# Performance work log

Hardware: AMD Instinct MI355X
Metric: run time of the kernel (lower is better)

The kernel has to match this reference:

```python
import jax, jax.numpy as jnp
import numpy as np

VOCAB, EMB, HID = 1000, 128, 256
B, T = 64, 1024


def setup_inputs() -> dict:
    key = jax.random.key(0)
    k1, k2, k3, k4, k5, k6, k7 = jax.random.split(key, 7)
    loading_lists = jax.random.randint(k1, (B, T), 0, VOCAB)
    lengths = jnp.maximum(jax.random.randint(k2, (B,), 0, T), 1)  # length >= 1 as in env
    s_ih = 1.0 / np.sqrt(HID)
    return {
        "loading_lists": loading_lists,
        "loading_list_lengths": lengths,
        "emb": jax.random.normal(k3, (VOCAB, EMB), dtype=jnp.float32),
        "W_ih": jax.random.uniform(k4, (4 * HID, EMB), minval=-s_ih, maxval=s_ih, dtype=jnp.float32),
        "W_hh": jax.random.uniform(k5, (4 * HID, HID), minval=-s_ih, maxval=s_ih, dtype=jnp.float32),
        "b_ih": jax.random.uniform(k6, (4 * HID,), minval=-s_ih, maxval=s_ih, dtype=jnp.float32),
        "b_hh": jax.random.uniform(k7, (4 * HID,), minval=-s_ih, maxval=s_ih, dtype=jnp.float32),
    }


def reference(loading_lists, loading_list_lengths, emb, W_ih, W_hh, b_ih, b_hh):
    # Embedding lookup: [B, T, E]
    x = emb[loading_lists]
    Bv, Tv, _ = x.shape
    H = W_hh.shape[1]
    # Precompute input projections for all timesteps: [B, T, 4H]
    xproj = jnp.einsum("bte,ge->btg", x, W_ih) + b_ih + b_hh
    xproj_t = jnp.swapaxes(xproj, 0, 1)  # [T, B, 4H]
    lengths = loading_list_lengths

    def step(carry, inp):
        h, c = carry
        xw_t, t = inp
        gates = xw_t + h @ W_hh.T  # [B, 4H]
        i_g, f_g, g_g, o_g = jnp.split(gates, 4, axis=-1)  # torch gate order i,f,g,o
        i_g = jax.nn.sigmoid(i_g)
        f_g = jax.nn.sigmoid(f_g)
        g_g = jnp.tanh(g_g)
        o_g = jax.nn.sigmoid(o_g)
        c_new = f_g * c + i_g * g_g
        h_new = o_g * jnp.tanh(c_new)
        valid = (t < lengths)[:, None]  # freeze state past each sample's length
        h = jnp.where(valid, h_new, h)
        c = jnp.where(valid, c_new, c)
        return (h, c), None

    h0 = jnp.zeros((Bv, H), dtype=x.dtype)
    c0 = jnp.zeros((Bv, H), dtype=x.dtype)
    (h_last, _), _ = jax.lax.scan(step, (h0, c0), (xproj_t, jnp.arange(Tv)))
    return h_last  # [B, H]
```

## Files before the change

kernel.cpp:

```cpp
#include <hip/hip_runtime.h>
#include <math.h>

#define VOCAB 1000
#define EMB   128
#define HID   256
#define G4    1024
#define BATCH 64
#define SEQT  1024
#define KVH   48
#define KLH   16

typedef unsigned int u32;
typedef _Float16 f16;
typedef __attribute__((ext_vector_type(2))) _Float16 h2v;
union H2U { u32 u; h2v h; unsigned short s[2]; };

#if defined(__has_builtin)
# if __has_builtin(__builtin_amdgcn_fdot2)
#  define HAVE_FDOT2 1
# endif
#endif
__device__ __forceinline__ float fdot2_(u32 a, u32 b, float c) {
    H2U ua, ub; ua.u = a; ub.u = b;
#ifdef HAVE_FDOT2
    return __builtin_amdgcn_fdot2(ua.h, ub.h, c, false);
#else
    return c + (float)ua.h.x * (float)ub.h.x + (float)ua.h.y * (float)ub.h.y;
#endif
}

__device__ __forceinline__ float sigmoidf_(float x) {
    return 1.f / (1.f + __expf(-x));
}
__device__ __forceinline__ float tanhf_(float x) {
    return 1.f - 2.f / (__expf(2.f * x) + 1.f);
}

__global__ __launch_bounds__(1024) void eproj_kernel(
    const float* __restrict__ emb, const float* __restrict__ W_ih,
    const float* __restrict__ b_ih, const float* __restrict__ b_hh,
    float* __restrict__ eproj)
{
    const int v0 = blockIdx.x * 8;
    const int g  = threadIdx.x;
    __shared__ __align__(16) float4 x_sh[8][EMB / 4];
    if (g < 256) {
        const int r = g >> 5, cc = g & 31;
        x_sh[r][cc] = ((const float4*)(emb + (size_t)(v0 + r) * EMB))[cc];
    }
    __syncthreads();
    const float4* wrow = (const float4*)(W_ih + (size_t)g * EMB);
    float a0[8], a1[8], a2[8], a3[8];
#pragma unroll
    for (int r = 0; r < 8; r++) { a0[r] = a1[r] = a2[r] = a3[r] = 0.f; }
#pragma unroll 4
    for (int e4 = 0; e4 < EMB / 4; e4++) {
        float4 wv = wrow[e4];
#pragma unroll
        for (int r = 0; r < 8; r++) {
            float4 xv = x_sh[r][e4];
            a0[r] += wv.x * xv.x;
            a1[r] += wv.y * xv.y;
            a2[r] += wv.z * xv.z;
            a3[r] += wv.w * xv.w;
        }
    }
    const float bias = b_ih[g] + b_hh[g];
#pragma unroll
    for (int r = 0; r < 8; r++)
        eproj[(size_t)(v0 + r) * G4 + g] =
            (a0[r] + a1[r]) + (a2[r] + a3[r]) + bias;
}

__global__ __launch_bounds__(128) void pack_whh(
    const float* __restrict__ Whh, u32* __restrict__ wvq, u32* __restrict__ wlq)
{
    const int r = blockIdx.x;
    const int m = threadIdx.x;
    H2U u;
    u.h.x = (f16)Whh[(size_t)r * HID + 2 * m];
    u.h.y = (f16)Whh[(size_t)r * HID + 2 * m + 1];
    const int j  = m >> 6;
    const int mm = m & 63;
    if (mm < KVH) {
        const int chunk = j * (KVH / 4) + (mm >> 2);
        wvq[(size_t)chunk * (G4 * 4) + r * 4 + (mm & 3)] = u.u;
    } else {
        const int t2 = mm - KVH;
        const int chunk = j * (KLH / 4) + (t2 >> 2);
        wlq[(size_t)chunk * (G4 * 4) + r * 4 + (t2 & 3)] = u.u;
    }
}

#define REG_CHUNK(q) do {                                                   \
    uint4 h4 = hb4[(q)];                                                    \
    aI = fdot2_(wI[4*(q)+0], h4.x, aI); aF = fdot2_(wF[4*(q)+0], h4.x, aF); \
    aG = fdot2_(wG[4*(q)+0], h4.x, aG); aO = fdot2_(wO[4*(q)+0], h4.x, aO); \
    aI = fdot2_(wI[4*(q)+1], h4.y, aI); aF = fdot2_(wF[4*(q)+1], h4.y, aF); \
    aG = fdot2_(wG[4*(q)+1], h4.y, aG); aO = fdot2_(wO[4*(q)+1], h4.y, aO); \
    aI = fdot2_(wI[4*(q)+2], h4.z, aI); aF = fdot2_(wF[4*(q)+2], h4.z, aF); \
    aG = fdot2_(wG[4*(q)+2], h4.z, aG); aO = fdot2_(wO[4*(q)+2], h4.z, aO); \
    aI = fdot2_(wI[4*(q)+3], h4.w, aI); aF = fdot2_(wF[4*(q)+3], h4.w, aF); \
    aG = fdot2_(wG[4*(q)+3], h4.w, aG); aO = fdot2_(wO[4*(q)+3], h4.w, aO); \
} while (0)

#define TAIL_CHUNK(q) do {                                                  \
    uint4 h4 = hb4[KVH / 4 + (q)];                                          \
    const int ch = j * (KLH / 4) + (q);                                     \
    uint4 tI = ((const uint4*)wl_sh)[ch * G4 + rI];                         \
    uint4 tF = ((const uint4*)wl_sh)[ch * G4 + rF];                         \
    uint4 tG = ((const uint4*)wl_sh)[ch * G4 + rG];                         \
    uint4 tO = ((const uint4*)wl_sh)[ch * G4 + rO];                         \
    aI = fdot2_(tI.x, h4.x, aI); aF = fdot2_(tF.x, h4.x, aF);               \
    aG = fdot2_(tG.x, h4.x, aG); aO = fdot2_(tO.x, h4.x, aO);               \
    aI = fdot2_(tI.y, h4.y, aI); aF = fdot2_(tF.y, h4.y, aF);               \
    aG = fdot2_(tG.y, h4.y, aG); aO = fdot2_(tO.y, h4.y, aO);               \
    aI = fdot2_(tI.z, h4.z, aI); aF = fdot2_(tF.z, h4.z, aF);               \
    aG = fdot2_(tG.z, h4.z, aG); aO = fdot2_(tO.z, h4.z, aO);               \
    aI = fdot2_(tI.w, h4.w, aI); aF = fdot2_(tF.w, h4.w, aF);               \
    aG = fdot2_(tG.w, h4.w, aG); aO = fdot2_(tO.w, h4.w, aO);               \
} while (0)

__global__ __launch_bounds__(512, 2) void lstm_single_cu(
    const int* __restrict__ ids, const int* __restrict__ lens,
    const float* __restrict__ eproj,
    const u32* __restrict__ wvq, const u32* __restrict__ wlq,
    float* __restrict__ out)
{
    const int b   = blockIdx.x;
    const int tau = threadIdx.x;
    const int u   = tau & (HID - 1);
    const int j   = tau >> 8;
    const int rI  = u;
    const int rF  = 256 + u;
    const int rG  = 512 + u;
    const int rO  = 768 + u;

    __shared__ u32    wl_sh[2 * (KLH / 4) * G4 * 4];
    __shared__ u32    h2_sh[2][HID / 2];
    __shared__ float4 gs4[HID];
    __shared__ int    id_sh[SEQT];

    const int* idr = ids + (size_t)b * SEQT;
    ((int2*)id_sh)[tau] = ((const int2*)idr)[tau];
    if (tau < HID / 2) h2_sh[0][tau] = 0u;

    {
        const uint4* src = (const uint4*)wlq;
        uint4*       dst = (uint4*)wl_sh;
#pragma unroll
        for (int t = 0; t < 2 * (KLH / 4) * G4 / 512; t++)
            dst[t * 512 + tau] = src[t * 512 + tau];
    }

    u32 wI[KVH], wF[KVH], wG[KVH], wO[KVH];
#pragma unroll
    for (int q = 0; q < KVH / 4; q++) {
        const int ch = j * (KVH / 4) + q;
        uint4 ti = ((const uint4*)wvq)[ch * G4 + rI];
        uint4 tf = ((const uint4*)wvq)[ch * G4 + rF];
        uint4 tg = ((const uint4*)wvq)[ch * G4 + rG];
        uint4 to = ((const uint4*)wvq)[ch * G4 + rO];
        wI[4 * q + 0] = ti.x; wI[4 * q + 1] = ti.y;
        wI[4 * q + 2] = ti.z; wI[4 * q + 3] = ti.w;
        wF[4 * q + 0] = tf.x; wF[4 * q + 1] = tf.y;
        wF[4 * q + 2] = tf.z; wF[4 * q + 3] = tf.w;
        wG[4 * q + 0] = tg.x; wG[4 * q + 1] = tg.y;
        wG[4 * q + 2] = tg.z; wG[4 * q + 3] = tg.w;
        wO[4 * q + 0] = to.x; wO[4 * q + 1] = to.y;
        wO[4 * q + 2] = to.z; wO[4 * q + 3] = to.w;
    }

    const int len = lens[b];
    float c = 0.f, hf = 0.f;

    float xI = 0.f, xF = 0.f, xG = 0.f, xO = 0.f;
    if (j == 0) {
        const float* e0 = eproj + (size_t)idr[0] * G4;
        xI = e0[rI]; xF = e0[rF]; xG = e0[rG]; xO = e0[rO];
    }

    __syncthreads();

    for (int t = 0; t < len; t++) {
        const int nt = (t + 1 < len) ? t + 1 : len - 1;
        const int nid = id_sh[nt];
        float nI = 0.f, nF = 0.f, nG = 0.f, nO = 0.f;
        if (j == 0) {
            const float* en = eproj + (size_t)nid * G4;
            nI = en[rI]; nF = en[rF]; nG = en[rG]; nO = en[rO];
        }

        const int p = t & 1;
        const uint4* hb4 = (const uint4*)h2_sh[p] + 16 * j;
        float aI = xI, aF = xF, aG = xG, aO = xO;

        if (j == 0) {
#pragma unroll
            for (int q = 0; q < KVH / 4; q++) REG_CHUNK(q);
#pragma unroll
            for (int q = 0; q < KLH / 4; q++) TAIL_CHUNK(q);
        } else {
#pragma unroll
            for (int q = 0; q < KLH / 4; q++) TAIL_CHUNK(q);
#pragma unroll
            for (int q = 0; q < KVH / 4; q++) REG_CHUNK(q);
        }

        if (j == 1) {
            gs4[u] = make_float4(aI, aF, aG, aO);
        }
        __syncthreads();

        if (j == 0) {
            float4 pp = gs4[u];
            float ig = sigmoidf_(aI + pp.x);
            float fg = sigmoidf_(aF + pp.y);
            float gg = tanhf_(aG + pp.z);
            float og = sigmoidf_(aO + pp.w);
            c  = fg * c + ig * gg;
            hf = og * tanhf_(c);
            H2U hv; hv.h.x = (f16)hf; hv.h.y = (f16)0.f;
            ((unsigned short*)h2_sh[p ^ 1])[u] = hv.s[0];
        }
        xI = nI; xF = nF; xG = nG; xO = nO;
        __syncthreads();
    }

    if (tau < HID) out[(size_t)b * HID + u] = hf;
}

__global__ __launch_bounds__(1024, 1) void lstm_fallback(
    const int* __restrict__ ids, const int* __restrict__ lens,
    const float* __restrict__ emb, const float* __restrict__ W_ih,
    const float* __restrict__ b_ih, const float* __restrict__ b_hh,
    const float* __restrict__ W_hh, float* __restrict__ out)
{
    const int b = blockIdx.x;
    const int t = threadIdx.x;

    __shared__ __align__(16) float h_sh[HID];
    __shared__ __align__(16) float c_sh[HID];
    __shared__ __align__(16) float gates[G4];
    __shared__ __align__(16) float x_sh[EMB];

    float wih[EMB];
    {
        const float4* wr = (const float4*)(W_ih + (size_t)t * EMB);
#pragma unroll
        for (int e4 = 0; e4 < EMB / 4; e4++) {
            float4 wv = wr[e4];
            wih[4 * e4 + 0] = wv.x;
            wih[4 * e4 + 1] = wv.y;
            wih[4 * e4 + 2] = wv.z;
            wih[4 * e4 + 3] = wv.w;
        }
    }
    float bias = b_ih[t] + b_hh[t];

    const int len = lens[b];
    const int* ids_row = ids + (size_t)b * SEQT;
    if (t < HID) { h_sh[t] = 0.f; c_sh[t] = 0.f; }
    __syncthreads();

    for (int step = 0; step < len; step++) {
        int id = ids_row[step];
        if (t < EMB / 4) {
            ((float4*)x_sh)[t] = ((const float4*)(emb + (size_t)id * EMB))[t];
        }
        __syncthreads();
        float a0 = bias, a1 = 0.f, a2 = 0.f, a3 = 0.f;
#pragma unroll
        for (int e4 = 0; e4 < EMB / 4; e4++) {
            float4 xv = ((const float4*)x_sh)[e4];
            a0 += wih[4 * e4 + 0] * xv.x;
            a1 += wih[4 * e4 + 1] * xv.y;
            a2 += wih[4 * e4 + 2] * xv.z;
            a3 += wih[4 * e4 + 3] * xv.w;
        }
        float acc = (a0 + a1) + (a2 + a3);

        const float* wrow = W_hh + (size_t)t * HID;
        a0 = acc; a1 = 0.f; a2 = 0.f; a3 = 0.f;
        for (int k4 = 0; k4 < HID / 4; k4++) {
            float4 hv = ((const float4*)h_sh)[k4];
            float4 wv = ((const float4*)wrow)[k4];
            a0 += wv.x * hv.x;
            a1 += wv.y * hv.y;
            a2 += wv.z * hv.z;
            a3 += wv.w * hv.w;
        }
        gates[t] = (a0 + a1) + (a2 + a3);
        __syncthreads();

        if (t < HID) {
            float ig = sigmoidf_(gates[t]);
            float fg = sigmoidf_(gates[HID + t]);
            float gg = tanhf_(gates[2 * HID + t]);
            float og = sigmoidf_(gates[3 * HID + t]);
            float cc = fg * c_sh[t] + ig * gg;
            c_sh[t] = cc;
            h_sh[t] = og * tanhf_(cc);
        }
        __syncthreads();
    }
    if (t < HID) out[(size_t)b * HID + t] = h_sh[t];
}

extern "C" void kernel_launch(void* const* d_in, const int* in_sizes, int n_in,
                              void* d_out, int out_size, void* d_ws, size_t ws_size,
                              hipStream_t stream) {
    const int*   ids  = (const int*)d_in[0];
    const int*   lens = (const int*)d_in[1];
    const float* emb  = (const float*)d_in[2];
    const float* Wih  = (const float*)d_in[3];
    const float* Whh  = (const float*)d_in[4];
    const float* bih  = (const float*)d_in[5];
    const float* bhh  = (const float*)d_in[6];
    float* out = (float*)d_out;

    const size_t ep_bytes = (size_t)VOCAB * G4 * sizeof(float);
    const size_t wv_off   = ep_bytes;
    const size_t wv_bytes = (size_t)2 * (KVH / 4) * G4 * 4 * sizeof(u32);
    const size_t wl_off   = wv_off + wv_bytes;
    const size_t wl_bytes = (size_t)2 * (KLH / 4) * G4 * 4 * sizeof(u32);

    if (ws_size >= wl_off + wl_bytes) {
        float* eproj = (float*)d_ws;
        u32*   wvp   = (u32*)((char*)d_ws + wv_off);
        u32*   wlp   = (u32*)((char*)d_ws + wl_off);
        eproj_kernel<<<VOCAB / 8, 1024, 0, stream>>>(emb, Wih, bih, bhh, eproj);
        pack_whh<<<G4, 128, 0, stream>>>(Whh, wvp, wlp);
        lstm_single_cu<<<BATCH, 512, 0, stream>>>(ids, lens, eproj, wvp, wlp, out);
    } else {
        lstm_fallback<<<BATCH, 1024, 0, stream>>>(
            ids, lens, emb, Wih, bih, bhh, Whh, out);
    }
}
```

Baseline: 1.568 ms.

## Stream part of W_hh tail from global/L2 instead of LDS each step

Splits the non-register portion of the recurrent weights into two halves: one stays in LDS, the other is reloaded from global memory (L2-resident) every timestep into registers, with the loads issued after the dot products so they overlap the gate/sync phase. This halves LDS weight traffic per step and shrinks LDS usage, possibly allowing more occupancy or fewer bank conflicts. The cost is per-step global loads and extra register pressure, and the branch-specific ordering of register vs LDS chunks is removed.

```diff
diff --git a/kernel.cpp b/kernel.cpp
--- a/kernel.cpp
+++ b/kernel.cpp
@@ -8,7 +8,8 @@
 #define BATCH 64
 #define SEQT  1024
 #define KVH   48
-#define KLH   16
+#define KLS   8
+#define KGH   8
 
 typedef unsigned int u32;
 typedef _Float16 f16;
@@ -73,7 +74,8 @@
 }
 
 __global__ __launch_bounds__(128) void pack_whh(
-    const float* __restrict__ Whh, u32* __restrict__ wvq, u32* __restrict__ wlq)
+    const float* __restrict__ Whh, u32* __restrict__ wvq,
+    u32* __restrict__ wlq, u32* __restrict__ wgq)
 {
     const int r = blockIdx.x;
     const int m = threadIdx.x;
@@ -85,10 +87,14 @@
     if (mm < KVH) {
         const int chunk = j * (KVH / 4) + (mm >> 2);
         wvq[(size_t)chunk * (G4 * 4) + r * 4 + (mm & 3)] = u.u;
+    } else if (mm < KVH + KLS) {
+        const int t2 = mm - KVH;
+        const int chunk = j * (KLS / 4) + (t2 >> 2);
+        wlq[(size_t)chunk * (G4 * 4) + r * 4 + (t2 & 3)] = u.u;
     } else {
-        const int t2 = mm - KVH;
-        const int chunk = j * (KLH / 4) + (t2 >> 2);
-        wlq[(size_t)chunk * (G4 * 4) + r * 4 + (t2 & 3)] = u.u;
+        const int t2 = mm - KVH - KLS;
+        const int chunk = j * (KGH / 4) + (t2 >> 2);
+        wgq[(size_t)chunk * (G4 * 4) + r * 4 + (t2 & 3)] = u.u;
     }
 }
 
@@ -104,28 +110,23 @@
     aG = fdot2_(wG[4*(q)+3], h4.w, aG); aO = fdot2_(wO[4*(q)+3], h4.w, aO); \
 } while (0)
 
-#define TAIL_CHUNK(q) do {                                                  \
-    uint4 h4 = hb4[KVH / 4 + (q)];                                          \
-    const int ch = j * (KLH / 4) + (q);                                     \
-    uint4 tI = ((const uint4*)wl_sh)[ch * G4 + rI];                         \
-    uint4 tF = ((const uint4*)wl_sh)[ch * G4 + rF];                         \
-    uint4 tG = ((const uint4*)wl_sh)[ch * G4 + rG];                         \
-    uint4 tO = ((const uint4*)wl_sh)[ch * G4 + rO];                         \
-    aI = fdot2_(tI.x, h4.x, aI); aF = fdot2_(tF.x, h4.x, aF);               \
-    aG = fdot2_(tG.x, h4.x, aG); aO = fdot2_(tO.x, h4.x, aO);               \
-    aI = fdot2_(tI.y, h4.y, aI); aF = fdot2_(tF.y, h4.y, aF);               \
-    aG = fdot2_(tG.y, h4.y, aG); aO = fdot2_(tO.y, h4.y, aO);               \
-    aI = fdot2_(tI.z, h4.z, aI); aF = fdot2_(tF.z, h4.z, aF);               \
-    aG = fdot2_(tG.z, h4.z, aG); aO = fdot2_(tO.z, h4.z, aO);               \
-    aI = fdot2_(tI.w, h4.w, aI); aF = fdot2_(tF.w, h4.w, aF);               \
-    aG = fdot2_(tG.w, h4.w, aG); aO = fdot2_(tO.w, h4.w, aO);               \
+#define VAL_CHUNK(tI, tF, tG, tO, hq) do {                                  \
+    uint4 h4 = hb4[(hq)];                                                   \
+    aI = fdot2_((tI).x, h4.x, aI); aF = fdot2_((tF).x, h4.x, aF);           \
+    aG = fdot2_((tG).x, h4.x, aG); aO = fdot2_((tO).x, h4.x, aO);           \
+    aI = fdot2_((tI).y, h4.y, aI); aF = fdot2_((tF).y, h4.y, aF);           \
+    aG = fdot2_((tG).y, h4.y, aG); aO = fdot2_((tO).y, h4.y, aO);           \
+    aI = fdot2_((tI).z, h4.z, aI); aF = fdot2_((tF).z, h4.z, aF);           \
+    aG = fdot2_((tG).z, h4.z, aG); aO = fdot2_((tO).z, h4.z, aO);           \
+    aI = fdot2_((tI).w, h4.w, aI); aF = fdot2_((tF).w, h4.w, aF);           \
+    aG = fdot2_((tG).w, h4.w, aG); aO = fdot2_((tO).w, h4.w, aO);           \
 } while (0)
 
 __global__ __launch_bounds__(512, 2) void lstm_single_cu(
     const int* __restrict__ ids, const int* __restrict__ lens,
     const float* __restrict__ eproj,
     const u32* __restrict__ wvq, const u32* __restrict__ wlq,
-    float* __restrict__ out)
+    const u32* __restrict__ wgq, float* __restrict__ out)
 {
     const int b   = blockIdx.x;
     const int tau = threadIdx.x;
@@ -136,7 +137,7 @@
     const int rG  = 512 + u;
     const int rO  = 768 + u;
 
-    __shared__ u32    wl_sh[2 * (KLH / 4) * G4 * 4];
+    __shared__ u32    wl_sh[4 * G4 * 4];
     __shared__ u32    h2_sh[2][HID / 2];
     __shared__ float4 gs4[HID];
     __shared__ int    id_sh[SEQT];
@@ -149,7 +150,7 @@
         const uint4* src = (const uint4*)wlq;
         uint4*       dst = (uint4*)wl_sh;
 #pragma unroll
-        for (int t = 0; t < 2 * (KLH / 4) * G4 / 512; t++)
+        for (int t = 0; t < 4 * G4 / 512; t++)
             dst[t * 512 + tau] = src[t * 512 + tau];
     }
 
@@ -171,6 +172,9 @@
         wO[4 * q + 2] = to.z; wO[4 * q + 3] = to.w;
     }
 
+    const uint4* g0 = (const uint4*)wgq + (size_t)(2 * j + 0) * G4;
+    const uint4* g1 = (const uint4*)wgq + (size_t)(2 * j + 1) * G4;
+
     const int len = lens[b];
     float c = 0.f, hf = 0.f;
 
@@ -179,6 +183,9 @@
         const float* e0 = eproj + (size_t)idr[0] * G4;
         xI = e0[rI]; xF = e0[rF]; xG = e0[rG]; xO = e0[rO];
     }
+
+    uint4 gi0 = g0[rI], gf0 = g0[rF], gg0 = g0[rG], go0 = g0[rO];
+    uint4 gi1 = g1[rI], gf1 = g1[rF], gg1 = g1[rG], go1 = g1[rO];
 
     __syncthreads();
 
@@ -195,17 +202,24 @@
         const uint4* hb4 = (const uint4*)h2_sh[p] + 16 * j;
         float aI = xI, aF = xF, aG = xG, aO = xO;
 
-        if (j == 0) {
-#pragma unroll
-            for (int q = 0; q < KVH / 4; q++) REG_CHUNK(q);
-#pragma unroll
-            for (int q = 0; q < KLH / 4; q++) TAIL_CHUNK(q);
-        } else {
-#pragma unroll
-            for (int q = 0; q < KLH / 4; q++) TAIL_CHUNK(q);
-#pragma unroll
-            for (int q = 0; q < KVH / 4; q++) REG_CHUNK(q);
-        }
+        VAL_CHUNK(gi0, gf0, gg0, go0, 14);
+        VAL_CHUNK(gi1, gf1, gg1, go1, 15);
+
+#pragma unroll
+        for (int q = 0; q < KVH / 4; q++) REG_CHUNK(q);
+
+#pragma unroll
+        for (int q = 0; q < KLS / 4; q++) {
+            const int ch = j * (KLS / 4) + q;
+            uint4 tI = ((const uint4*)wl_sh)[ch * G4 + rI];
+            uint4 tF = ((const uint4*)wl_sh)[ch * G4 + rF];
+            uint4 tG = ((const uint4*)wl_sh)[ch * G4 + rG];
+            uint4 tO = ((const uint4*)wl_sh)[ch * G4 + rO];
+            VAL_CHUNK(tI, tF, tG, tO, KVH / 4 + q);
+        }
+
+        gi0 = g0[rI]; gf0 = g0[rF]; gg0 = g0[rG]; go0 = g0[rO];
+        gi1 = g1[rI]; gf1 = g1[rF]; gg1 = g1[rG]; go1 = g1[rO];
 
         if (j == 1) {
             gs4[u] = make_float4(aI, aF, aG, aO);
@@ -216,9 +230,9 @@
             float4 pp = gs4[u];
             float ig = sigmoidf_(aI + pp.x);
             float fg = sigmoidf_(aF + pp.y);
-            float gg = tanhf_(aG + pp.z);
+            float gg2 = tanhf_(aG + pp.z);
             float og = sigmoidf_(aO + pp.w);
-            c  = fg * c + ig * gg;
+            c  = fg * c + ig * gg2;
             hf = og * tanhf_(c);
             H2U hv; hv.h.x = (f16)hf; hv.h.y = (f16)0.f;
             ((unsigned short*)h2_sh[p ^ 1])[u] = hv.s[0];
@@ -323,15 +337,19 @@
     const size_t wv_off   = ep_bytes;
     const size_t wv_bytes = (size_t)2 * (KVH / 4) * G4 * 4 * sizeof(u32);
     const size_t wl_off   = wv_off + wv_bytes;
-    const size_t wl_bytes = (size_t)2 * (KLH / 4) * G4 * 4 * sizeof(u32);
-
-    if (ws_size >= wl_off + wl_bytes) {
+    const size_t wl_bytes = (size_t)2 * (KLS / 4) * G4 * 4 * sizeof(u32);
+    const size_t wg_off   = wl_off + wl_bytes;
+    const size_t wg_bytes = (size_t)2 * (KGH / 4) * G4 * 4 * sizeof(u32);
+
+    if (ws_size >= wg_off + wg_bytes) {
         float* eproj = (float*)d_ws;
         u32*   wvp   = (u32*)((char*)d_ws + wv_off);
         u32*   wlp   = (u32*)((char*)d_ws + wl_off);
+        u32*   wgp   = (u32*)((char*)d_ws + wg_off);
         eproj_kernel<<<VOCAB / 8, 1024, 0, stream>>>(emb, Wih, bih, bhh, eproj);
-        pack_whh<<<G4, 128, 0, stream>>>(Whh, wvp, wlp);
-        lstm_single_cu<<<BATCH, 512, 0, stream>>>(ids, lens, eproj, wvp, wlp, out);
+        pack_whh<<<G4, 128, 0, stream>>>(Whh, wvp, wlp, wgp);
+        lstm_single_cu<<<BATCH, 512, 0, stream>>>(
+            ids, lens, eproj, wvp, wlp, wgp, out);
     } else {
         lstm_fallback<<<BATCH, 1024, 0, stream>>>(
             ids, lens, emb, Wih, bih, bhh, Whh, out);
```

Measured after the change: 1.563 ms (median of 2 runs). About the same (-0.3%).
